# Performance work log

Measured on AMD Instinct MI355X. Metric: run time of the kernel, lower is better.

Reference implementation:

```python
import jax, jax.numpy as jnp
import numpy as np

NUM_HEADS = 8
KEY_DIM = 64
WINDOW = 8
SHIFT = 4
B, H, W, C = 8, 64, 64, 512


def setup_inputs() -> dict:
    key = jax.random.key(0)
    ks = jax.random.split(key, 6)
    s = 0.02  # small init scale for numerically tame attention
    return {
        "x": jax.random.normal(ks[0], (B, H, W, C), jnp.float32),
        "wq": jax.random.normal(ks[1], (C, NUM_HEADS, KEY_DIM), jnp.float32) * s,
        "bq": jnp.zeros((NUM_HEADS, KEY_DIM), jnp.float32),
        "wk": jax.random.normal(ks[2], (C, NUM_HEADS, KEY_DIM), jnp.float32) * s,
        "bk": jnp.zeros((NUM_HEADS, KEY_DIM), jnp.float32),
        "wv": jax.random.normal(ks[3], (C, NUM_HEADS, KEY_DIM), jnp.float32) * s,
        "bv": jnp.zeros((NUM_HEADS, KEY_DIM), jnp.float32),
        "wo": jax.random.normal(ks[4], (NUM_HEADS, KEY_DIM, C), jnp.float32) * s,
        "bo": jnp.zeros((C,), jnp.float32),
    }


def reference(x, wq, bq, wk, bk, wv, bv, wo, bo):
    b, h, w, c = x.shape
    ws, ss = WINDOW, SHIFT
    pad_h = (ws - h % ws) % ws
    pad_w = (ws - w % ws) % ws
    padded = jnp.pad(x, ((0, 0), (0, pad_h), (0, pad_w), (0, 0)))
    if ss:
        padded = jnp.roll(padded, shift=(-ss, -ss), axis=(1, 2))
    ph, pw = h + pad_h, w + pad_w
    nh, nw = ph // ws, pw // ws
    # window partition: [B, nh, ws, nw, ws, C] -> [B*nh*nw, ws*ws, C]
    win = padded.reshape(b, nh, ws, nw, ws, c)
    win = win.transpose(0, 1, 3, 2, 4, 5).reshape(-1, ws * ws, c)
    q = jnp.einsum("ntc,chd->nthd", win, wq) + bq
    k = jnp.einsum("ntc,chd->nthd", win, wk) + bk
    v = jnp.einsum("ntc,chd->nthd", win, wv) + bv
    scale = 1.0 / jnp.sqrt(jnp.asarray(KEY_DIM, q.dtype))
    scores = jnp.einsum("nqhd,nkhd->nhqk", q, k) * scale
    attn = jax.nn.softmax(scores, axis=-1)
    out = jnp.einsum("nhqk,nkhd->nqhd", attn, v)
    proj = jnp.einsum("nqhd,hdc->nqc", out, wo) + bo
    # window merge
    merged = proj.reshape(b, nh, nw, ws, ws, c)
    merged = merged.transpose(0, 1, 3, 2, 4, 5).reshape(b, ph, pw, c)
    if ss:
        merged = jnp.roll(merged, shift=(ss, ss), axis=(1, 2))
    if pad_h or pad_w:
        merged = merged[:, :h, :w, :]
    return x + merged
```

## Files before the change

### kernel.cpp

```cpp
#include <hip/hip_runtime.h>

typedef unsigned short u16;
typedef short bf16x8 __attribute__((ext_vector_type(8)));
typedef float f32x4 __attribute__((ext_vector_type(4)));

typedef __attribute__((address_space(3))) unsigned int lds_uint;
typedef __attribute__((address_space(1))) const unsigned int glob_uint;

__device__ __forceinline__ void gll16(const void* g, void* l) {
    __builtin_amdgcn_global_load_lds((glob_uint*)g, (lds_uint*)l, 16, 0, 0);
}

__device__ __forceinline__ u16 f2b(float f) {
    union { float f; unsigned int u; } cv; cv.f = f;
    unsigned int u = cv.u;
    u += 0x7fffu + ((u >> 16) & 1u);
    return (u16)(u >> 16);
}

__global__ void prep_kernel(const float* __restrict__ wq, const float* __restrict__ wk,
                            const float* __restrict__ wv, const float* __restrict__ wo,
                            const float* __restrict__ bq, const float* __restrict__ bk,
                            const float* __restrict__ bv,
                            u16* __restrict__ wqkvT, u16* __restrict__ woT,
                            float* __restrict__ biasq) {
    int idx = blockIdx.x * 256 + threadIdx.x;
    const int N1 = 512 * 1536;
    const int N2 = 512 * 512;
    if (idx < N1) {
        int k = idx / 1536, n = idx % 1536;
        int which = n >> 9, nn = n & 511;
        const float* w = (which == 0) ? wq : (which == 1) ? wk : wv;
        wqkvT[n * 512 + k] = f2b(w[k * 512 + nn]);
    } else if (idx < N1 + N2) {
        int j = idx - N1;
        int k = j / 512, n = j % 512;
        woT[n * 512 + k] = f2b(wo[k * 512 + n]);
    } else if (idx < N1 + N2 + 1536) {
        int n = idx - N1 - N2;
        biasq[n] = (n < 512) ? bq[n] : (n < 1024) ? bk[n - 512] : bv[n - 1024];
    }
}

__global__ __launch_bounds__(256) void pre_kernel(const float* __restrict__ x,
                                                  u16* __restrict__ xw) {
    int idx = blockIdx.x * 256 + threadIdx.x;
    int row = idx >> 6;
    int c = (idx & 63) * 8;
    int b_ = row >> 12, win = (row >> 6) & 63, t = row & 63;
    int wi = win >> 3, wj = win & 7, ti = t >> 3, tj = t & 7;
    int hh = (wi * 8 + ti + 4) & 63, ww = (wj * 8 + tj + 4) & 63;
    const float* src = x + ((size_t)b_ * 4096 + hh * 64 + ww) * 512 + c;
    float4 v0 = *(const float4*)src;
    float4 v1 = *(const float4*)(src + 4);
    ushort4 p0, p1;
    p0.x = f2b(v0.x); p0.y = f2b(v0.y); p0.z = f2b(v0.z); p0.w = f2b(v0.w);
    p1.x = f2b(v1.x); p1.y = f2b(v1.y); p1.z = f2b(v1.z); p1.w = f2b(v1.w);
    u16* dst = xw + (size_t)row * 512 + c;
    *(ushort4*)dst = p0;
    *(ushort4*)(dst + 4) = p1;
}

__global__ __launch_bounds__(256) void qkv_gemm(const u16* __restrict__ xw,
        const u16* __restrict__ wqkvT, const float* __restrict__ biasq,
        u16* __restrict__ qkvb) {
    __shared__ u16 As[128 * 64];
    __shared__ u16 Bs[128 * 64];
    const int tid = threadIdx.x;
    const int lane = tid & 63, wid = tid >> 6;
    const int wr = wid >> 1, wc = wid & 1;
    const int m = lane & 15, qd = lane >> 4;
    const int rowBase = blockIdx.y * 128;
    const int colBase = blockIdx.x * 128;
    const int c8 = (lane & 7) ^ (lane >> 3);

    f32x4 acc[4][4];
#pragma unroll
    for (int i = 0; i < 4; ++i)
#pragma unroll
        for (int j = 0; j < 4; ++j) acc[i][j] = (f32x4){0.f, 0.f, 0.f, 0.f};

    for (int kt = 0; kt < 8; ++kt) {
        const int k0 = kt * 64;
        __syncthreads();
#pragma unroll
        for (int j = 0; j < 4; ++j) {
            int q = (j * 4 + wid) * 64 + lane;
            int r = (j * 4 + wid) * 8 + (lane >> 3);
            gll16(xw + (size_t)(rowBase + r) * 512 + k0 + c8 * 8, &As[q * 8]);
            gll16(wqkvT + (size_t)(colBase + r) * 512 + k0 + c8 * 8, &Bs[q * 8]);
        }
        __syncthreads();
#pragma unroll
        for (int s = 0; s < 2; ++s) {
            bf16x8 a[4], b[4];
#pragma unroll
            for (int ni = 0; ni < 4; ++ni) {
                int R = wc * 64 + ni * 16 + m;
                b[ni] = *(const bf16x8*)&Bs[R * 64 + (((s * 4 + qd) ^ (R & 7)) * 8)];
            }
#pragma unroll
            for (int mi = 0; mi < 4; ++mi) {
                int R = wr * 64 + mi * 16 + m;
                a[mi] = *(const bf16x8*)&As[R * 64 + (((s * 4 + qd) ^ (R & 7)) * 8)];
            }
#pragma unroll
            for (int mi = 0; mi < 4; ++mi)
#pragma unroll
                for (int ni = 0; ni < 4; ++ni)
                    acc[mi][ni] = __builtin_amdgcn_mfma_f32_16x16x32_bf16(a[mi], b[ni], acc[mi][ni], 0, 0, 0);
        }
    }

    float bias[4];
#pragma unroll
    for (int ni = 0; ni < 4; ++ni) bias[ni] = biasq[colBase + wc * 64 + ni * 16 + m];
#pragma unroll
    for (int mi = 0; mi < 4; ++mi) {
#pragma unroll
        for (int rr = 0; rr < 4; ++rr) {
            int row = rowBase + wr * 64 + mi * 16 + qd * 4 + rr;
            u16* dst = qkvb + (size_t)row * 1536 + colBase + wc * 64;
#pragma unroll
            for (int ni = 0; ni < 4; ++ni)
                dst[ni * 16 + m] = f2b(acc[mi][ni][rr] + bias[ni]);
        }
    }
}

__global__ __launch_bounds__(256) void attn_kernel(const u16* __restrict__ qkvb,
                                                   u16* __restrict__ ows) {
    __shared__ u16 Sb[4 * 64 * 72];
    const int tid = threadIdx.x, lane = tid & 63, wid = tid >> 6;
    const int task = blockIdx.x * 4 + wid;
    const int win = task >> 3, h = task & 7;
    const int m = lane & 15, qd = lane >> 4;
    const u16* base = qkvb + (size_t)win * 64 * 1536;
    u16* Sl = Sb + wid * 64 * 72;

    bf16x8 qa[4][2], ka[4][2];
#pragma unroll
    for (int mi = 0; mi < 4; ++mi)
#pragma unroll
        for (int s = 0; s < 2; ++s) {
            const u16* p = base + (size_t)(mi * 16 + m) * 1536 + h * 64 + s * 32 + qd * 8;
            qa[mi][s] = *(const bf16x8*)p;
            ka[mi][s] = *(const bf16x8*)(p + 512);
        }
    bf16x8 vr[8];
#pragma unroll
    for (int i = 0; i < 8; ++i) {
        int r = i * 8 + (lane >> 3);
        vr[i] = *(const bf16x8*)(base + (size_t)r * 1536 + 1024 + h * 64 + (lane & 7) * 8);
    }

    f32x4 sa[4][4];
#pragma unroll
    for (int i = 0; i < 4; ++i)
#pragma unroll
        for (int j = 0; j < 4; ++j) sa[i][j] = (f32x4){0.f, 0.f, 0.f, 0.f};
#pragma unroll
    for (int mi = 0; mi < 4; ++mi)
#pragma unroll
        for (int ni = 0; ni < 4; ++ni)
#pragma unroll
            for (int s = 0; s < 2; ++s)
                sa[mi][ni] = __builtin_amdgcn_mfma_f32_16x16x32_bf16(qa[mi][s], ka[ni][s], sa[mi][ni], 0, 0, 0);

    const float c1 = 0.125f * 1.4426950408889634f;
#pragma unroll
    for (int mi = 0; mi < 4; ++mi) {
#pragma unroll
        for (int rr = 0; rr < 4; ++rr) {
            float mx = -3.4e38f;
#pragma unroll
            for (int ni = 0; ni < 4; ++ni) mx = fmaxf(mx, sa[mi][ni][rr]);
            mx = fmaxf(mx, __shfl_xor(mx, 1, 64));
            mx = fmaxf(mx, __shfl_xor(mx, 2, 64));
            mx = fmaxf(mx, __shfl_xor(mx, 4, 64));
            mx = fmaxf(mx, __shfl_xor(mx, 8, 64));
            float sum = 0.f;
#pragma unroll
            for (int ni = 0; ni < 4; ++ni) {
                float p = exp2f((sa[mi][ni][rr] - mx) * c1);
                sa[mi][ni][rr] = p;
                sum += p;
            }
            sum += __shfl_xor(sum, 1, 64);
            sum += __shfl_xor(sum, 2, 64);
            sum += __shfl_xor(sum, 4, 64);
            sum += __shfl_xor(sum, 8, 64);
            float inv = 1.f / sum;
            int row = mi * 16 + qd * 4 + rr;
#pragma unroll
            for (int ni = 0; ni < 4; ++ni)
                Sl[row * 72 + ni * 16 + m] = f2b(sa[mi][ni][rr] * inv);
        }
    }

    bf16x8 pa[4][2];
#pragma unroll
    for (int mi = 0; mi < 4; ++mi)
#pragma unroll
        for (int s = 0; s < 2; ++s)
            pa[mi][s] = *(const bf16x8*)&Sl[(mi * 16 + m) * 72 + s * 32 + qd * 8];

#pragma unroll
    for (int i = 0; i < 8; ++i) {
        int r = i * 8 + (lane >> 3);
        *(bf16x8*)&Sl[r * 72 + (lane & 7) * 8] = vr[i];
    }
    f32x4 oa[4][4];
#pragma unroll
    for (int i = 0; i < 4; ++i)
#pragma unroll
        for (int j = 0; j < 4; ++j) oa[i][j] = (f32x4){0.f, 0.f, 0.f, 0.f};
#pragma unroll
    for (int ni = 0; ni < 4; ++ni)
#pragma unroll
        for (int s = 0; s < 2; ++s) {
            bf16x8 v;
#pragma unroll
            for (int j = 0; j < 8; ++j)
                ((short*)&v)[j] = (short)Sl[(s * 32 + qd * 8 + j) * 72 + ni * 16 + m];
#pragma unroll
            for (int mi = 0; mi < 4; ++mi)
                oa[mi][ni] = __builtin_amdgcn_mfma_f32_16x16x32_bf16(pa[mi][s], v, oa[mi][ni], 0, 0, 0);
        }

#pragma unroll
    for (int mi = 0; mi < 4; ++mi)
#pragma unroll
        for (int rr = 0; rr < 4; ++rr) {
            int t = mi * 16 + qd * 4 + rr;
            u16* dst = ows + (size_t)(win * 64 + t) * 512 + h * 64;
#pragma unroll
            for (int ni = 0; ni < 4; ++ni)
                dst[ni * 16 + m] = f2b(oa[mi][ni][rr]);
        }
}

__global__ __launch_bounds__(256) void proj_gemm(const u16* __restrict__ ows,
        const u16* __restrict__ woT, const float* __restrict__ bo,
        const float* __restrict__ x, float* __restrict__ out) {
    __shared__ u16 As[128 * 64];
    __shared__ u16 Bs[128 * 64];
    const int tid = threadIdx.x;
    const int lane = tid & 63, wid = tid >> 6;
    const int wr = wid >> 1, wc = wid & 1;
    const int m = lane & 15, qd = lane >> 4;
    const int rowBase = blockIdx.y * 128;
    const int colBase = blockIdx.x * 128;
    const int c8 = (lane & 7) ^ (lane >> 3);

    f32x4 acc[4][4];
#pragma unroll
    for (int i = 0; i < 4; ++i)
#pragma unroll
        for (int j = 0; j < 4; ++j) acc[i][j] = (f32x4){0.f, 0.f, 0.f, 0.f};

    for (int kt = 0; kt < 8; ++kt) {
        const int k0 = kt * 64;
        __syncthreads();
#pragma unroll
        for (int j = 0; j < 4; ++j) {
            int q = (j * 4 + wid) * 64 + lane;
            int r = (j * 4 + wid) * 8 + (lane >> 3);
            gll16(ows + (size_t)(rowBase + r) * 512 + k0 + c8 * 8, &As[q * 8]);
            gll16(woT + (size_t)(colBase + r) * 512 + k0 + c8 * 8, &Bs[q * 8]);
        }
        __syncthreads();
#pragma unroll
        for (int s = 0; s < 2; ++s) {
            bf16x8 a[4], b[4];
#pragma unroll
            for (int ni = 0; ni < 4; ++ni) {
                int R = wc * 64 + ni * 16 + m;
                b[ni] = *(const bf16x8*)&Bs[R * 64 + (((s * 4 + qd) ^ (R & 7)) * 8)];
            }
#pragma unroll
            for (int mi = 0; mi < 4; ++mi) {
                int R = wr * 64 + mi * 16 + m;
                a[mi] = *(const bf16x8*)&As[R * 64 + (((s * 4 + qd) ^ (R & 7)) * 8)];
            }
#pragma unroll
            for (int mi = 0; mi < 4; ++mi)
#pragma unroll
                for (int ni = 0; ni < 4; ++ni)
                    acc[mi][ni] = __builtin_amdgcn_mfma_f32_16x16x32_bf16(a[mi], b[ni], acc[mi][ni], 0, 0, 0);
        }
    }

#pragma unroll
    for (int mi = 0; mi < 4; ++mi) {
#pragma unroll
        for (int rr = 0; rr < 4; ++rr) {
            int row = rowBase + wr * 64 + mi * 16 + qd * 4 + rr;
            int win = row >> 6, t = row & 63;
            int b_ = win >> 6, wh = (win >> 3) & 7, ww_ = win & 7;
            int ti = t >> 3, tj = t & 7;
            int hh = (wh * 8 + ti + 4) & 63;
            int www = (ww_ * 8 + tj + 4) & 63;
            size_t tok = (size_t)b_ * 4096 + hh * 64 + www;
#pragma unroll
            for (int ni = 0; ni < 4; ++ni) {
                int col = colBase + wc * 64 + ni * 16 + m;
                out[tok * 512 + col] = acc[mi][ni][rr] + bo[col] + x[tok * 512 + col];
            }
        }
    }
}

extern "C" void kernel_launch(void* const* d_in, const int* in_sizes, int n_in,
                              void* d_out, int out_size, void* d_ws, size_t ws_size,
                              hipStream_t stream) {
    const float* x  = (const float*)d_in[0];
    const float* wq = (const float*)d_in[1];
    const float* bq = (const float*)d_in[2];
    const float* wk = (const float*)d_in[3];
    const float* bk = (const float*)d_in[4];
    const float* wv = (const float*)d_in[5];
    const float* bv = (const float*)d_in[6];
    const float* wo = (const float*)d_in[7];
    const float* bo = (const float*)d_in[8];
    float* out = (float*)d_out;
    char* ws = (char*)d_ws;

    u16*   wqkvT = (u16*)ws;
    u16*   woT   = (u16*)(ws + 1572864);
    float* biasq = (float*)(ws + 1572864 + 524288);
    size_t off = 2103296;
    u16* xw   = (u16*)(ws + off);
    u16* qkvb = xw + (size_t)16777216;
    u16* ows  = xw;

    const int prepN = 512 * 1536 + 512 * 512 + 1536;
    prep_kernel<<<dim3((prepN + 255) / 256), dim3(256), 0, stream>>>(
        wq, wk, wv, wo, bq, bk, bv, wqkvT, woT, biasq);
    pre_kernel<<<dim3(8192), dim3(256), 0, stream>>>(x, xw);
    qkv_gemm<<<dim3(12, 256), dim3(256), 0, stream>>>(xw, wqkvT, biasq, qkvb);
    attn_kernel<<<dim3(1024), dim3(256), 0, stream>>>(qkvb, ows);
    proj_gemm<<<dim3(4, 256), dim3(256), 0, stream>>>(ows, woT, bo, x, out);
}
```

Measured before the change: 278.3 us.

## Fuse QKV projection with per-window attention, keeping Q/K/V in LDS

Replaces the separate QKV GEMM and attention kernels with one kernel per window. Each block loops over the 8 heads, computing that head's Q, K and V tile in LDS and running attention on it directly, so the 1536-wide QKV intermediate never goes to global memory. Weights are regrouped per head and the MFMA operands are swapped so outputs can be stored as packed vectors. The projection epilogue now reads and writes float4. The costs: only 512 blocks, each reloading the x tile for every head, and heavier LDS usage, which may reduce occupancy.

```diff
diff --git a/kernel.cpp b/kernel.cpp
--- a/kernel.cpp
+++ b/kernel.cpp
@@ -18,27 +18,36 @@
     return (u16)(u >> 16);
 }
 
+__device__ __forceinline__ uint2 pack4(float a, float b, float c, float d) {
+    uint2 r;
+    r.x = (unsigned int)f2b(a) | ((unsigned int)f2b(b) << 16);
+    r.y = (unsigned int)f2b(c) | ((unsigned int)f2b(d) << 16);
+    return r;
+}
+
 __global__ void prep_kernel(const float* __restrict__ wq, const float* __restrict__ wk,
                             const float* __restrict__ wv, const float* __restrict__ wo,
                             const float* __restrict__ bq, const float* __restrict__ bk,
                             const float* __restrict__ bv,
-                            u16* __restrict__ wqkvT, u16* __restrict__ woT,
-                            float* __restrict__ biasq) {
+                            u16* __restrict__ wqkvh, u16* __restrict__ woT,
+                            float* __restrict__ biash) {
     int idx = blockIdx.x * 256 + threadIdx.x;
     const int N1 = 512 * 1536;
     const int N2 = 512 * 512;
     if (idx < N1) {
-        int k = idx / 1536, n = idx % 1536;
-        int which = n >> 9, nn = n & 511;
-        const float* w = (which == 0) ? wq : (which == 1) ? wk : wv;
-        wqkvT[n * 512 + k] = f2b(w[k * 512 + nn]);
+        int k = idx / 1536, n2 = idx % 1536;
+        int h = n2 / 192, j = n2 % 192;
+        const float* w = (j < 64) ? wq : (j < 128) ? wk : wv;
+        wqkvh[(size_t)n2 * 512 + k] = f2b(w[k * 512 + h * 64 + (j & 63)]);
     } else if (idx < N1 + N2) {
-        int j = idx - N1;
-        int k = j / 512, n = j % 512;
+        int i = idx - N1;
+        int k = i / 512, n = i % 512;
         woT[n * 512 + k] = f2b(wo[k * 512 + n]);
     } else if (idx < N1 + N2 + 1536) {
-        int n = idx - N1 - N2;
-        biasq[n] = (n < 512) ? bq[n] : (n < 1024) ? bk[n - 512] : bv[n - 1024];
+        int n2 = idx - N1 - N2;
+        int h = n2 / 192, j = n2 % 192;
+        const float* b = (j < 64) ? bq : (j < 128) ? bk : bv;
+        biash[n2] = b[h * 64 + (j & 63)];
     }
 }
 
@@ -61,120 +70,109 @@
     *(ushort4*)(dst + 4) = p1;
 }
 
-__global__ __launch_bounds__(256) void qkv_gemm(const u16* __restrict__ xw,
-        const u16* __restrict__ wqkvT, const float* __restrict__ biasq,
-        u16* __restrict__ qkvb) {
-    __shared__ u16 As[128 * 64];
-    __shared__ u16 Bs[128 * 64];
+__global__ __launch_bounds__(256) void fused_qkv_attn(const u16* __restrict__ xw,
+        const u16* __restrict__ wqkvh, const float* __restrict__ biash,
+        u16* __restrict__ ows) {
+    __shared__ u16 S[29696];
     const int tid = threadIdx.x;
     const int lane = tid & 63, wid = tid >> 6;
     const int wr = wid >> 1, wc = wid & 1;
     const int m = lane & 15, qd = lane >> 4;
-    const int rowBase = blockIdx.y * 128;
-    const int colBase = blockIdx.x * 128;
-    const int c8 = (lane & 7) ^ (lane >> 3);
-
-    f32x4 acc[4][4];
-#pragma unroll
-    for (int i = 0; i < 4; ++i)
-#pragma unroll
-        for (int j = 0; j < 4; ++j) acc[i][j] = (f32x4){0.f, 0.f, 0.f, 0.f};
-
-    for (int kt = 0; kt < 8; ++kt) {
-        const int k0 = kt * 64;
+    const int win = blockIdx.x;
+    const int rowBase = win * 64;
+
+    u16* As  = S;
+    u16* Bs  = S + 4096;
+    u16* QKs = S + 16384;
+    u16* VT  = S + 25088;
+    u16* Pw  = S + wid * 2176;
+
+    for (int h = 0; h < 8; ++h) {
+        const u16* Bsrc = wqkvh + (size_t)h * 192 * 512;
+        f32x4 acc[2][6];
+#pragma unroll
+        for (int i = 0; i < 2; ++i)
+#pragma unroll
+            for (int j = 0; j < 6; ++j) acc[i][j] = (f32x4){0.f, 0.f, 0.f, 0.f};
+
+        for (int kt = 0; kt < 8; ++kt) {
+            const int k0 = kt * 64;
+            __syncthreads();
+#pragma unroll
+            for (int j = 0; j < 2; ++j) {
+                int q = j * 256 + tid;
+                int r = q >> 3, c = (q & 7) ^ (r & 7);
+                gll16(xw + (size_t)(rowBase + r) * 512 + k0 + c * 8, As + q * 8);
+            }
+#pragma unroll
+            for (int j = 0; j < 6; ++j) {
+                int q = j * 256 + tid;
+                int r = q >> 3, c = (q & 7) ^ (r & 7);
+                gll16(Bsrc + (size_t)r * 512 + k0 + c * 8, Bs + q * 8);
+            }
+            __syncthreads();
+#pragma unroll
+            for (int s = 0; s < 2; ++s) {
+                bf16x8 a[2], b[6];
+#pragma unroll
+                for (int ni = 0; ni < 6; ++ni) {
+                    int R = wc * 96 + ni * 16 + m;
+                    b[ni] = *(const bf16x8*)&Bs[R * 64 + (((s * 4 + qd) ^ (R & 7)) * 8)];
+                }
+#pragma unroll
+                for (int mi = 0; mi < 2; ++mi) {
+                    int R = wr * 32 + mi * 16 + m;
+                    a[mi] = *(const bf16x8*)&As[R * 64 + (((s * 4 + qd) ^ (R & 7)) * 8)];
+                }
+#pragma unroll
+                for (int mi = 0; mi < 2; ++mi)
+#pragma unroll
+                    for (int ni = 0; ni < 6; ++ni)
+                        acc[mi][ni] = __builtin_amdgcn_mfma_f32_16x16x32_bf16(b[ni], a[mi], acc[mi][ni], 0, 0, 0);
+            }
+        }
+
+#pragma unroll
+        for (int mi = 0; mi < 2; ++mi) {
+            int t = wr * 32 + mi * 16 + m;
+#pragma unroll
+            for (int ni = 0; ni < 6; ++ni) {
+                int cn = wc * 96 + ni * 16;
+                float4 bb = *(const float4*)&biash[h * 192 + cn + qd * 4];
+                if (cn < 128) {
+                    *(uint2*)&QKs[t * 136 + cn + qd * 4] =
+                        pack4(acc[mi][ni][0] + bb.x, acc[mi][ni][1] + bb.y,
+                              acc[mi][ni][2] + bb.z, acc[mi][ni][3] + bb.w);
+                } else {
+                    int d0 = cn - 128 + qd * 4;
+                    VT[(d0 + 0) * 72 + t] = f2b(acc[mi][ni][0] + bb.x);
+                    VT[(d0 + 1) * 72 + t] = f2b(acc[mi][ni][1] + bb.y);
+                    VT[(d0 + 2) * 72 + t] = f2b(acc[mi][ni][2] + bb.z);
+                    VT[(d0 + 3) * 72 + t] = f2b(acc[mi][ni][3] + bb.w);
+                }
+            }
+        }
         __syncthreads();
-#pragma unroll
-        for (int j = 0; j < 4; ++j) {
-            int q = (j * 4 + wid) * 64 + lane;
-            int r = (j * 4 + wid) * 8 + (lane >> 3);
-            gll16(xw + (size_t)(rowBase + r) * 512 + k0 + c8 * 8, &As[q * 8]);
-            gll16(wqkvT + (size_t)(colBase + r) * 512 + k0 + c8 * 8, &Bs[q * 8]);
-        }
-        __syncthreads();
+
+        const int q0 = wid * 16;
+        f32x4 sa[4];
+#pragma unroll
+        for (int ni = 0; ni < 4; ++ni) sa[ni] = (f32x4){0.f, 0.f, 0.f, 0.f};
 #pragma unroll
         for (int s = 0; s < 2; ++s) {
-            bf16x8 a[4], b[4];
+            bf16x8 qf = *(const bf16x8*)&QKs[(q0 + m) * 136 + s * 32 + qd * 8];
 #pragma unroll
             for (int ni = 0; ni < 4; ++ni) {
-                int R = wc * 64 + ni * 16 + m;
-                b[ni] = *(const bf16x8*)&Bs[R * 64 + (((s * 4 + qd) ^ (R & 7)) * 8)];
-            }
-#pragma unroll
-            for (int mi = 0; mi < 4; ++mi) {
-                int R = wr * 64 + mi * 16 + m;
-                a[mi] = *(const bf16x8*)&As[R * 64 + (((s * 4 + qd) ^ (R & 7)) * 8)];
-            }
-#pragma unroll
-            for (int mi = 0; mi < 4; ++mi)
-#pragma unroll
-                for (int ni = 0; ni < 4; ++ni)
-                    acc[mi][ni] = __builtin_amdgcn_mfma_f32_16x16x32_bf16(a[mi], b[ni], acc[mi][ni], 0, 0, 0);
-        }
-    }
-
-    float bias[4];
-#pragma unroll
-    for (int ni = 0; ni < 4; ++ni) bias[ni] = biasq[colBase + wc * 64 + ni * 16 + m];
-#pragma unroll
-    for (int mi = 0; mi < 4; ++mi) {
-#pragma unroll
-        for (int rr = 0; rr < 4; ++rr) {
-            int row = rowBase + wr * 64 + mi * 16 + qd * 4 + rr;
-            u16* dst = qkvb + (size_t)row * 1536 + colBase + wc * 64;
-#pragma unroll
-            for (int ni = 0; ni < 4; ++ni)
-                dst[ni * 16 + m] = f2b(acc[mi][ni][rr] + bias[ni]);
-        }
-    }
-}
-
-__global__ __launch_bounds__(256) void attn_kernel(const u16* __restrict__ qkvb,
-                                                   u16* __restrict__ ows) {
-    __shared__ u16 Sb[4 * 64 * 72];
-    const int tid = threadIdx.x, lane = tid & 63, wid = tid >> 6;
-    const int task = blockIdx.x * 4 + wid;
-    const int win = task >> 3, h = task & 7;
-    const int m = lane & 15, qd = lane >> 4;
-    const u16* base = qkvb + (size_t)win * 64 * 1536;
-    u16* Sl = Sb + wid * 64 * 72;
-
-    bf16x8 qa[4][2], ka[4][2];
-#pragma unroll
-    for (int mi = 0; mi < 4; ++mi)
-#pragma unroll
-        for (int s = 0; s < 2; ++s) {
-            const u16* p = base + (size_t)(mi * 16 + m) * 1536 + h * 64 + s * 32 + qd * 8;
-            qa[mi][s] = *(const bf16x8*)p;
-            ka[mi][s] = *(const bf16x8*)(p + 512);
-        }
-    bf16x8 vr[8];
-#pragma unroll
-    for (int i = 0; i < 8; ++i) {
-        int r = i * 8 + (lane >> 3);
-        vr[i] = *(const bf16x8*)(base + (size_t)r * 1536 + 1024 + h * 64 + (lane & 7) * 8);
-    }
-
-    f32x4 sa[4][4];
-#pragma unroll
-    for (int i = 0; i < 4; ++i)
-#pragma unroll
-        for (int j = 0; j < 4; ++j) sa[i][j] = (f32x4){0.f, 0.f, 0.f, 0.f};
-#pragma unroll
-    for (int mi = 0; mi < 4; ++mi)
-#pragma unroll
-        for (int ni = 0; ni < 4; ++ni)
-#pragma unroll
-            for (int s = 0; s < 2; ++s)
-                sa[mi][ni] = __builtin_amdgcn_mfma_f32_16x16x32_bf16(qa[mi][s], ka[ni][s], sa[mi][ni], 0, 0, 0);
-
-    const float c1 = 0.125f * 1.4426950408889634f;
-#pragma unroll
-    for (int mi = 0; mi < 4; ++mi) {
+                bf16x8 kf = *(const bf16x8*)&QKs[(ni * 16 + m) * 136 + 64 + s * 32 + qd * 8];
+                sa[ni] = __builtin_amdgcn_mfma_f32_16x16x32_bf16(qf, kf, sa[ni], 0, 0, 0);
+            }
+        }
+        const float c1 = 0.125f * 1.4426950408889634f;
 #pragma unroll
         for (int rr = 0; rr < 4; ++rr) {
             float mx = -3.4e38f;
 #pragma unroll
-            for (int ni = 0; ni < 4; ++ni) mx = fmaxf(mx, sa[mi][ni][rr]);
+            for (int ni = 0; ni < 4; ++ni) mx = fmaxf(mx, sa[ni][rr]);
             mx = fmaxf(mx, __shfl_xor(mx, 1, 64));
             mx = fmaxf(mx, __shfl_xor(mx, 2, 64));
             mx = fmaxf(mx, __shfl_xor(mx, 4, 64));
@@ -182,8 +180,8 @@
             float sum = 0.f;
 #pragma unroll
             for (int ni = 0; ni < 4; ++ni) {
-                float p = exp2f((sa[mi][ni][rr] - mx) * c1);
-                sa[mi][ni][rr] = p;
+                float p = exp2f((sa[ni][rr] - mx) * c1);
+                sa[ni][rr] = p;
                 sum += p;
             }
             sum += __shfl_xor(sum, 1, 64);
@@ -191,53 +189,30 @@
             sum += __shfl_xor(sum, 4, 64);
             sum += __shfl_xor(sum, 8, 64);
             float inv = 1.f / sum;
-            int row = mi * 16 + qd * 4 + rr;
+            int r = qd * 4 + rr;
 #pragma unroll
             for (int ni = 0; ni < 4; ++ni)
-                Sl[row * 72 + ni * 16 + m] = f2b(sa[mi][ni][rr] * inv);
-        }
+                Pw[r * 136 + ni * 16 + m] = f2b(sa[ni][rr] * inv);
+        }
+
+        f32x4 oa[4];
+#pragma unroll
+        for (int ni = 0; ni < 4; ++ni) oa[ni] = (f32x4){0.f, 0.f, 0.f, 0.f};
+#pragma unroll
+        for (int s = 0; s < 2; ++s) {
+            bf16x8 pf = *(const bf16x8*)&Pw[m * 136 + s * 32 + qd * 8];
+#pragma unroll
+            for (int ni = 0; ni < 4; ++ni) {
+                bf16x8 vf = *(const bf16x8*)&VT[(ni * 16 + m) * 72 + s * 32 + qd * 8];
+                oa[ni] = __builtin_amdgcn_mfma_f32_16x16x32_bf16(vf, pf, oa[ni], 0, 0, 0);
+            }
+        }
+        u16* dst = ows + (size_t)(rowBase + q0 + m) * 512 + h * 64;
+#pragma unroll
+        for (int ni = 0; ni < 4; ++ni)
+            *(uint2*)&dst[ni * 16 + qd * 4] =
+                pack4(oa[ni][0], oa[ni][1], oa[ni][2], oa[ni][3]);
     }
-
-    bf16x8 pa[4][2];
-#pragma unroll
-    for (int mi = 0; mi < 4; ++mi)
-#pragma unroll
-        for (int s = 0; s < 2; ++s)
-            pa[mi][s] = *(const bf16x8*)&Sl[(mi * 16 + m) * 72 + s * 32 + qd * 8];
-
-#pragma unroll
-    for (int i = 0; i < 8; ++i) {
-        int r = i * 8 + (lane >> 3);
-        *(bf16x8*)&Sl[r * 72 + (lane & 7) * 8] = vr[i];
-    }
-    f32x4 oa[4][4];
-#pragma unroll
-    for (int i = 0; i < 4; ++i)
-#pragma unroll
-        for (int j = 0; j < 4; ++j) oa[i][j] = (f32x4){0.f, 0.f, 0.f, 0.f};
-#pragma unroll
-    for (int ni = 0; ni < 4; ++ni)
-#pragma unroll
-        for (int s = 0; s < 2; ++s) {
-            bf16x8 v;
-#pragma unroll
-            for (int j = 0; j < 8; ++j)
-                ((short*)&v)[j] = (short)Sl[(s * 32 + qd * 8 + j) * 72 + ni * 16 + m];
-#pragma unroll
-            for (int mi = 0; mi < 4; ++mi)
-                oa[mi][ni] = __builtin_amdgcn_mfma_f32_16x16x32_bf16(pa[mi][s], v, oa[mi][ni], 0, 0, 0);
-        }
-
-#pragma unroll
-    for (int mi = 0; mi < 4; ++mi)
-#pragma unroll
-        for (int rr = 0; rr < 4; ++rr) {
-            int t = mi * 16 + qd * 4 + rr;
-            u16* dst = ows + (size_t)(win * 64 + t) * 512 + h * 64;
-#pragma unroll
-            for (int ni = 0; ni < 4; ++ni)
-                dst[ni * 16 + m] = f2b(oa[mi][ni][rr]);
-        }
 }
 
 __global__ __launch_bounds__(256) void proj_gemm(const u16* __restrict__ ows,
@@ -287,26 +262,30 @@
             for (int mi = 0; mi < 4; ++mi)
 #pragma unroll
                 for (int ni = 0; ni < 4; ++ni)
-                    acc[mi][ni] = __builtin_amdgcn_mfma_f32_16x16x32_bf16(a[mi], b[ni], acc[mi][ni], 0, 0, 0);
+                    acc[mi][ni] = __builtin_amdgcn_mfma_f32_16x16x32_bf16(b[ni], a[mi], acc[mi][ni], 0, 0, 0);
         }
     }
 
 #pragma unroll
     for (int mi = 0; mi < 4; ++mi) {
-#pragma unroll
-        for (int rr = 0; rr < 4; ++rr) {
-            int row = rowBase + wr * 64 + mi * 16 + qd * 4 + rr;
-            int win = row >> 6, t = row & 63;
-            int b_ = win >> 6, wh = (win >> 3) & 7, ww_ = win & 7;
-            int ti = t >> 3, tj = t & 7;
-            int hh = (wh * 8 + ti + 4) & 63;
-            int www = (ww_ * 8 + tj + 4) & 63;
-            size_t tok = (size_t)b_ * 4096 + hh * 64 + www;
-#pragma unroll
-            for (int ni = 0; ni < 4; ++ni) {
-                int col = colBase + wc * 64 + ni * 16 + m;
-                out[tok * 512 + col] = acc[mi][ni][rr] + bo[col] + x[tok * 512 + col];
-            }
+        int row = rowBase + wr * 64 + mi * 16 + m;
+        int win = row >> 6, t = row & 63;
+        int b_ = win >> 6, wh = (win >> 3) & 7, ww_ = win & 7;
+        int ti = t >> 3, tj = t & 7;
+        int hh = (wh * 8 + ti + 4) & 63;
+        int www = (ww_ * 8 + tj + 4) & 63;
+        size_t tok = (size_t)b_ * 4096 + hh * 64 + www;
+#pragma unroll
+        for (int ni = 0; ni < 4; ++ni) {
+            int col0 = colBase + wc * 64 + ni * 16 + qd * 4;
+            float4 xv = *(const float4*)&x[tok * 512 + col0];
+            float4 bv = *(const float4*)&bo[col0];
+            float4 o;
+            o.x = acc[mi][ni][0] + bv.x + xv.x;
+            o.y = acc[mi][ni][1] + bv.y + xv.y;
+            o.z = acc[mi][ni][2] + bv.z + xv.z;
+            o.w = acc[mi][ni][3] + bv.w + xv.w;
+            *(float4*)&out[tok * 512 + col0] = o;
         }
     }
 }
@@ -326,19 +305,17 @@
     float* out = (float*)d_out;
     char* ws = (char*)d_ws;
 
-    u16*   wqkvT = (u16*)ws;
+    u16*   wqkvh = (u16*)ws;
     u16*   woT   = (u16*)(ws + 1572864);
-    float* biasq = (float*)(ws + 1572864 + 524288);
+    float* biash = (float*)(ws + 1572864 + 524288);
     size_t off = 2103296;
-    u16* xw   = (u16*)(ws + off);
-    u16* qkvb = xw + (size_t)16777216;
-    u16* ows  = xw;
+    u16* xw  = (u16*)(ws + off);
+    u16* ows = xw + (size_t)16777216;
 
     const int prepN = 512 * 1536 + 512 * 512 + 1536;
     prep_kernel<<<dim3((prepN + 255) / 256), dim3(256), 0, stream>>>(
-        wq, wk, wv, wo, bq, bk, bv, wqkvT, woT, biasq);
+        wq, wk, wv, wo, bq, bk, bv, wqkvh, woT, biash);
     pre_kernel<<<dim3(8192), dim3(256), 0, stream>>>(x, xw);
-    qkv_gemm<<<dim3(12, 256), dim3(256), 0, stream>>>(xw, wqkvT, biasq, qkvb);
-    attn_kernel<<<dim3(1024), dim3(256), 0, stream>>>(qkvb, ows);
+    fused_qkv_attn<<<dim3(512), dim3(256), 0, stream>>>(xw, wqkvh, biash, ows);
     proj_gemm<<<dim3(4, 256), dim3(256), 0, stream>>>(ows, woT, bo, x, out);
 }
```

New measurement: 275.6 us. About the same (-1.0%).

## Vectorize GEMM and attention epilogues via swapped MFMA operands and LDS staging

Applied to the files above, without the earlier changes.

The QKV and projection GEMMs swap their MFMA operands so each lane holds four consecutive output columns. The results are then staged through swizzled LDS and written back as 16-byte coalesced stores instead of scattered 2- and 4-byte stores. Both GEMMs use a 1D grid remapped so that the eight blocks dispatched together land on different row groups, aiming at better XCD/L2 locality. The attention kernel loads V transposed into LDS so the PV MFMA operand is a single vector read, and it writes packed bf16 output. The cost is extra LDS round trips and barriers in the epilogues, plus bank-conflict-prone scalar transpose stores.

```diff
diff --git a/kernel.cpp b/kernel.cpp
--- a/kernel.cpp
+++ b/kernel.cpp
@@ -16,6 +16,13 @@
     unsigned int u = cv.u;
     u += 0x7fffu + ((u >> 16) & 1u);
     return (u16)(u >> 16);
+}
+
+__device__ __forceinline__ uint2 pack4(float a, float b, float c, float d) {
+    uint2 r;
+    r.x = (unsigned int)f2b(a) | ((unsigned int)f2b(b) << 16);
+    r.y = (unsigned int)f2b(c) | ((unsigned int)f2b(d) << 16);
+    return r;
 }
 
 __global__ void prep_kernel(const float* __restrict__ wq, const float* __restrict__ wk,
@@ -64,14 +71,17 @@
 __global__ __launch_bounds__(256) void qkv_gemm(const u16* __restrict__ xw,
         const u16* __restrict__ wqkvT, const float* __restrict__ biasq,
         u16* __restrict__ qkvb) {
-    __shared__ u16 As[128 * 64];
-    __shared__ u16 Bs[128 * 64];
+    __shared__ u16 S[16384];
+    u16* As = S;
+    u16* Bs = S + 8192;
     const int tid = threadIdx.x;
     const int lane = tid & 63, wid = tid >> 6;
     const int wr = wid >> 1, wc = wid & 1;
     const int m = lane & 15, qd = lane >> 4;
-    const int rowBase = blockIdx.y * 128;
-    const int colBase = blockIdx.x * 128;
+    const int g = blockIdx.x >> 3, x8 = blockIdx.x & 7;
+    const int bx = g % 12, by = g / 12 + x8 * 32;
+    const int rowBase = by * 128;
+    const int colBase = bx * 128;
     const int c8 = (lane & 7) ^ (lane >> 3);
 
     f32x4 acc[4][4];
@@ -108,22 +118,33 @@
             for (int mi = 0; mi < 4; ++mi)
 #pragma unroll
                 for (int ni = 0; ni < 4; ++ni)
-                    acc[mi][ni] = __builtin_amdgcn_mfma_f32_16x16x32_bf16(a[mi], b[ni], acc[mi][ni], 0, 0, 0);
-        }
-    }
-
-    float bias[4];
-#pragma unroll
-    for (int ni = 0; ni < 4; ++ni) bias[ni] = biasq[colBase + wc * 64 + ni * 16 + m];
+                    acc[mi][ni] = __builtin_amdgcn_mfma_f32_16x16x32_bf16(b[ni], a[mi], acc[mi][ni], 0, 0, 0);
+        }
+    }
+
+    __syncthreads();
 #pragma unroll
     for (int mi = 0; mi < 4; ++mi) {
-#pragma unroll
-        for (int rr = 0; rr < 4; ++rr) {
-            int row = rowBase + wr * 64 + mi * 16 + qd * 4 + rr;
-            u16* dst = qkvb + (size_t)row * 1536 + colBase + wc * 64;
-#pragma unroll
-            for (int ni = 0; ni < 4; ++ni)
-                dst[ni * 16 + m] = f2b(acc[mi][ni][rr] + bias[ni]);
+        int r = wr * 64 + mi * 16 + m;
+#pragma unroll
+        for (int ni = 0; ni < 4; ++ni) {
+            int ch = wc * 8 + ni * 2 + (qd >> 1);
+            float4 bb = *(const float4*)&biasq[colBase + wc * 64 + ni * 16 + qd * 4];
+            uint2 pk = pack4(acc[mi][ni][0] + bb.x, acc[mi][ni][1] + bb.y,
+                             acc[mi][ni][2] + bb.z, acc[mi][ni][3] + bb.w);
+            *(uint2*)&S[r * 128 + ((ch ^ (r & 15)) * 8) + (qd & 1) * 4] = pk;
+        }
+    }
+    __syncthreads();
+#pragma unroll
+    for (int it = 0; it < 4; ++it) {
+        int r = it * 32 + (tid >> 3);
+        int cb = (tid & 7) * 2;
+#pragma unroll
+        for (int cc = 0; cc < 2; ++cc) {
+            int pc = (cb + cc) ^ (r & 15);
+            uint4 v = *(const uint4*)&S[r * 128 + pc * 8];
+            *(uint4*)&qkvb[(size_t)(rowBase + r) * 1536 + colBase + (cb + cc) * 8] = v;
         }
     }
 }
@@ -147,12 +168,6 @@
             qa[mi][s] = *(const bf16x8*)p;
             ka[mi][s] = *(const bf16x8*)(p + 512);
         }
-    bf16x8 vr[8];
-#pragma unroll
-    for (int i = 0; i < 8; ++i) {
-        int r = i * 8 + (lane >> 3);
-        vr[i] = *(const bf16x8*)(base + (size_t)r * 1536 + 1024 + h * 64 + (lane & 7) * 8);
-    }
 
     f32x4 sa[4][4];
 #pragma unroll
@@ -206,10 +221,18 @@
             pa[mi][s] = *(const bf16x8*)&Sl[(mi * 16 + m) * 72 + s * 32 + qd * 8];
 
 #pragma unroll
-    for (int i = 0; i < 8; ++i) {
-        int r = i * 8 + (lane >> 3);
-        *(bf16x8*)&Sl[r * 72 + (lane & 7) * 8] = vr[i];
-    }
+    for (int it = 0; it < 4; ++it) {
+        int t = it * 16 + m;
+        const u16* vp = base + (size_t)t * 1536 + 1024 + h * 64 + qd * 16;
+        bf16x8 v0 = *(const bf16x8*)vp;
+        bf16x8 v1 = *(const bf16x8*)(vp + 8);
+#pragma unroll
+        for (int k = 0; k < 8; ++k) {
+            Sl[(qd * 16 + k) * 72 + t] = ((const u16*)&v0)[k];
+            Sl[(qd * 16 + 8 + k) * 72 + t] = ((const u16*)&v1)[k];
+        }
+    }
+
     f32x4 oa[4][4];
 #pragma unroll
     for (int i = 0; i < 4; ++i)
@@ -219,38 +242,36 @@
     for (int ni = 0; ni < 4; ++ni)
 #pragma unroll
         for (int s = 0; s < 2; ++s) {
-            bf16x8 v;
-#pragma unroll
-            for (int j = 0; j < 8; ++j)
-                ((short*)&v)[j] = (short)Sl[(s * 32 + qd * 8 + j) * 72 + ni * 16 + m];
+            bf16x8 vf = *(const bf16x8*)&Sl[(ni * 16 + m) * 72 + s * 32 + qd * 8];
 #pragma unroll
             for (int mi = 0; mi < 4; ++mi)
-                oa[mi][ni] = __builtin_amdgcn_mfma_f32_16x16x32_bf16(pa[mi][s], v, oa[mi][ni], 0, 0, 0);
-        }
-
-#pragma unroll
-    for (int mi = 0; mi < 4; ++mi)
-#pragma unroll
-        for (int rr = 0; rr < 4; ++rr) {
-            int t = mi * 16 + qd * 4 + rr;
-            u16* dst = ows + (size_t)(win * 64 + t) * 512 + h * 64;
-#pragma unroll
-            for (int ni = 0; ni < 4; ++ni)
-                dst[ni * 16 + m] = f2b(oa[mi][ni][rr]);
-        }
+                oa[mi][ni] = __builtin_amdgcn_mfma_f32_16x16x32_bf16(vf, pa[mi][s], oa[mi][ni], 0, 0, 0);
+        }
+
+#pragma unroll
+    for (int mi = 0; mi < 4; ++mi) {
+        u16* dst = ows + (size_t)(win * 64 + mi * 16 + m) * 512 + h * 64;
+#pragma unroll
+        for (int ni = 0; ni < 4; ++ni)
+            *(uint2*)&dst[ni * 16 + qd * 4] =
+                pack4(oa[mi][ni][0], oa[mi][ni][1], oa[mi][ni][2], oa[mi][ni][3]);
+    }
 }
 
 __global__ __launch_bounds__(256) void proj_gemm(const u16* __restrict__ ows,
         const u16* __restrict__ woT, const float* __restrict__ bo,
         const float* __restrict__ x, float* __restrict__ out) {
-    __shared__ u16 As[128 * 64];
-    __shared__ u16 Bs[128 * 64];
+    __shared__ float Sf[8192];
+    u16* As = (u16*)Sf;
+    u16* Bs = (u16*)Sf + 8192;
     const int tid = threadIdx.x;
     const int lane = tid & 63, wid = tid >> 6;
     const int wr = wid >> 1, wc = wid & 1;
     const int m = lane & 15, qd = lane >> 4;
-    const int rowBase = blockIdx.y * 128;
-    const int colBase = blockIdx.x * 128;
+    const int g = blockIdx.x >> 3, x8 = blockIdx.x & 7;
+    const int bx = g & 3, by = (g >> 2) + x8 * 32;
+    const int rowBase = by * 128;
+    const int colBase = bx * 128;
     const int c8 = (lane & 7) ^ (lane >> 3);
 
     f32x4 acc[4][4];
@@ -287,25 +308,48 @@
             for (int mi = 0; mi < 4; ++mi)
 #pragma unroll
                 for (int ni = 0; ni < 4; ++ni)
-                    acc[mi][ni] = __builtin_amdgcn_mfma_f32_16x16x32_bf16(a[mi], b[ni], acc[mi][ni], 0, 0, 0);
-        }
-    }
-
-#pragma unroll
-    for (int mi = 0; mi < 4; ++mi) {
-#pragma unroll
-        for (int rr = 0; rr < 4; ++rr) {
-            int row = rowBase + wr * 64 + mi * 16 + qd * 4 + rr;
-            int win = row >> 6, t = row & 63;
+                    acc[mi][ni] = __builtin_amdgcn_mfma_f32_16x16x32_bf16(b[ni], a[mi], acc[mi][ni], 0, 0, 0);
+        }
+    }
+
+#pragma unroll
+    for (int p = 0; p < 2; ++p) {
+        __syncthreads();
+        if (wr == p) {
+#pragma unroll
+            for (int mi = 0; mi < 4; ++mi) {
+                int row = mi * 16 + m;
+#pragma unroll
+                for (int ni = 0; ni < 4; ++ni) {
+                    int c = wc * 16 + ni * 4 + qd;
+                    *(f32x4*)&Sf[row * 128 + ((c ^ (row & 7)) * 4)] = acc[mi][ni];
+                }
+            }
+        }
+        __syncthreads();
+#pragma unroll
+        for (int sub = 0; sub < 2; ++sub) {
+            int row = sub * 32 + (tid >> 3);
+            int rowg = rowBase + p * 64 + row;
+            int win = rowg >> 6, t = rowg & 63;
             int b_ = win >> 6, wh = (win >> 3) & 7, ww_ = win & 7;
             int ti = t >> 3, tj = t & 7;
             int hh = (wh * 8 + ti + 4) & 63;
             int www = (ww_ * 8 + tj + 4) & 63;
             size_t tok = (size_t)b_ * 4096 + hh * 64 + www;
 #pragma unroll
-            for (int ni = 0; ni < 4; ++ni) {
-                int col = colBase + wc * 64 + ni * 16 + m;
-                out[tok * 512 + col] = acc[mi][ni][rr] + bo[col] + x[tok * 512 + col];
+            for (int j = 0; j < 4; ++j) {
+                int c = (tid & 7) * 4 + j;
+                f32x4 v = *(const f32x4*)&Sf[row * 128 + ((c ^ (row & 7)) * 4)];
+                int col0 = colBase + c * 4;
+                float4 bv = *(const float4*)&bo[col0];
+                float4 xv = *(const float4*)&x[tok * 512 + col0];
+                float4 o;
+                o.x = v[0] + bv.x + xv.x;
+                o.y = v[1] + bv.y + xv.y;
+                o.z = v[2] + bv.z + xv.z;
+                o.w = v[3] + bv.w + xv.w;
+                *(float4*)&out[tok * 512 + col0] = o;
             }
         }
     }
@@ -338,7 +382,7 @@
     prep_kernel<<<dim3((prepN + 255) / 256), dim3(256), 0, stream>>>(
         wq, wk, wv, wo, bq, bk, bv, wqkvT, woT, biasq);
     pre_kernel<<<dim3(8192), dim3(256), 0, stream>>>(x, xw);
-    qkv_gemm<<<dim3(12, 256), dim3(256), 0, stream>>>(xw, wqkvT, biasq, qkvb);
+    qkv_gemm<<<dim3(3072), dim3(256), 0, stream>>>(xw, wqkvT, biasq, qkvb);
     attn_kernel<<<dim3(1024), dim3(256), 0, stream>>>(qkvb, ows);
-    proj_gemm<<<dim3(4, 256), dim3(256), 0, stream>>>(ows, woT, bo, x, out);
-}
+    proj_gemm<<<dim3(1024), dim3(256), 0, stream>>>(ows, woT, bo, x, out);
+}
```

Result: no change. 282.1 us (+1.4%).
